# Kernel optimization log

Hardware: AMD Instinct MI355X
Metric: run time of the kernel (lower is better)

## Reference

```python
import jax, jax.numpy as jnp
import numpy as np

IN_CAPS, IN_SIZE = 1152, 8
OUT_CAPS, OUT_SIZE = 10, 16
ROUTING_ITERS = 3
EPS = 1e-8


def squash(s, axis):
    # v = (||s||^2 / (1 + ||s||^2)) * s / ||s||
    sq = jnp.sum(s * s, axis=axis, keepdims=True)
    return (sq / (1.0 + sq)) * s / jnp.sqrt(sq + EPS)


def setup_inputs() -> dict:
    key = jax.random.key(0)
    k1, k2 = jax.random.split(key)
    B = 1024
    x = jax.random.normal(k1, (B, IN_CAPS, IN_SIZE), dtype=jnp.float32)
    W = jax.random.normal(k2, (IN_CAPS, IN_SIZE, OUT_CAPS * OUT_SIZE), dtype=jnp.float32)
    b_ij = jnp.zeros((IN_CAPS, OUT_CAPS), dtype=jnp.float32)
    return {"x": x, "W": W, "b_ij": b_ij}


def reference(x, W, b_ij):
    B = x.shape[0]
    # u_hat[b,i,j,d]: prediction vectors. (B,1152,8) x (1152,8,160) -> (B,1152,160)
    u_hat = jnp.einsum('bis,iso->bio', x, W).reshape(B, IN_CAPS, OUT_CAPS, OUT_SIZE)
    u_hat_d = jax.lax.stop_gradient(u_hat)

    # initial coupling from learned logits b_ij
    c_ij = jax.nn.softmax(b_ij, axis=1)                      # (1152,10)
    s_j = jnp.einsum('ij,bijd->bjd', c_ij, u_hat_d)          # (B,10,16)
    v_j = squash(s_j, axis=2)

    b_batch = jnp.broadcast_to(b_ij, (B, IN_CAPS, OUT_CAPS))
    for it in range(ROUTING_ITERS):
        # agreement: (B,1152,10)
        b_batch = b_batch + jnp.einsum('bijd,bjd->bij', u_hat_d, v_j)
        c = jax.nn.softmax(b_batch, axis=2)                  # (B,1152,10)
        u = u_hat if it == ROUTING_ITERS - 1 else u_hat_d
        s_j = jnp.einsum('bij,bijd->bjd', c, u)              # (B,10,16)
        v_j = squash(s_j, axis=2)
    return v_j
```

## Files before the change

### kernel.cpp

```cpp
#include <hip/hip_runtime.h>

#define IC 1152
#define IS 8
#define OC 10
#define OS 16
#define OD 160
#define SQ_EPS 1e-8f

typedef _Float16 half8 __attribute__((ext_vector_type(8)));
typedef float f32x4 __attribute__((ext_vector_type(4)));


__global__ __launch_bounds__(160) void prep_w(const float* __restrict__ W,
                                              uint4* __restrict__ WF) {
  int cap = blockIdx.x;
  int j = threadIdx.x >> 4;
  int lp = threadIdx.x & 15;
  union { _Float16 h[8]; uint4 u; } pk;
#pragma unroll
  for (int i = 0; i < 8; i++)
    pk.h[i] = (_Float16)W[(size_t)cap * (IS * OD) + i * OD + j * 16 + lp];
  WF[((size_t)cap * OC + j) * 16 + lp] = pk.u;
}

template <bool PASS0>
__global__ __launch_bounds__(256) void pass_mfma(
    const float* __restrict__ x, const uint4* __restrict__ WF,
    const float* __restrict__ bij, const float* __restrict__ Vsum,
    float* __restrict__ s_accum, int Bn) {
  int b0 = blockIdx.x * 16;
  int cap0 = blockIdx.y * 64;
  int tid = threadIdx.x;
  int wid = tid >> 6;
  int lane = tid & 63;
  int bl = lane & 15;
  int og = (lane >> 4) * 4;
  int gb = b0 + bl;
  bool bok = gb < Bn;

  __shared__ __align__(16) uint4 xlh[64 * 16];
  __shared__ float sred[4 * 16 * 161];

  for (int e = tid; e < 64 * 16; e += 256) {
    int cc = e & 63, bb = e >> 6;
    int b = b0 + bb;
    float xf[8] = {0, 0, 0, 0, 0, 0, 0, 0};
    if (b < Bn) {
      *(float4*)&xf[0] = *(const float4*)&x[((size_t)b * IC + cap0 + cc) * IS];
      *(float4*)&xf[4] =
          *(const float4*)&x[((size_t)b * IC + cap0 + cc) * IS + 4];
    }
    union { _Float16 h[8]; uint4 u; } pk;
#pragma unroll
    for (int s = 0; s < 8; s++) pk.h[s] = (_Float16)xf[s];
    xlh[cc * 16 + (bb ^ (cc & 15))] = pk.u;
  }
  __syncthreads();

  f32x4 vs4[OC];
#pragma unroll
  for (int j = 0; j < OC; j++) vs4[j] = (f32x4){0.f, 0.f, 0.f, 0.f};
  if (!PASS0 && bok) {
    const float* vrow = Vsum + (size_t)gb * OD;
#pragma unroll
    for (int j = 0; j < OC; j++) {
      float4 t = *(const float4*)(vrow + j * 16 + og);
      vs4[j] = (f32x4){t.x, t.y, t.z, t.w};
    }
  }

  f32x4 sacc[OC];
#pragma unroll
  for (int j = 0; j < OC; j++) sacc[j] = (f32x4){0.f, 0.f, 0.f, 0.f};

  for (int c = 0; c < 16; ++c) {
    int cc = wid * 16 + c;
    int cap = cap0 + cc;

    union { uint4 u; half8 h; } xb;
    xb.u = xlh[cc * 16 + ((lane < 16 ? lane : 0) ^ (cc & 15))];
    if (lane >= 16) xb.u = make_uint4(0, 0, 0, 0);

    f32x4 uf[OC];
#pragma unroll
    for (int j = 0; j < OC; j++) {
      union { uint4 u; half8 h; } wa;
      wa.u = WF[((size_t)cap * OC + j) * 16 + (lane & 15)];
      if (lane >= 16) wa.u = make_uint4(0, 0, 0, 0);
      f32x4 z = {0.f, 0.f, 0.f, 0.f};
      uf[j] = __builtin_amdgcn_mfma_f32_16x16x32_f16(wa.h, xb.h, z, 0, 0, 0);
    }

    float l[OC];
#pragma unroll
    for (int j = 0; j < OC; j++) {
      float bj = bij[cap * OC + j];
      if (PASS0) {
        l[j] = bj;
      } else {
        float t = uf[j].x * vs4[j].x + uf[j].y * vs4[j].y +
                  uf[j].z * vs4[j].z + uf[j].w * vs4[j].w;
        t += __shfl_xor(t, 16, 64);
        t += __shfl_xor(t, 32, 64);
        l[j] = bj + t;
      }
    }
    float m = l[0];
#pragma unroll
    for (int j = 1; j < OC; j++) m = fmaxf(m, l[j]);
    float sum = 0.f, cexp[OC];
#pragma unroll
    for (int j = 0; j < OC; j++) {
      cexp[j] = __expf(l[j] - m);
      sum += cexp[j];
    }
    float inv = 1.f / sum;
#pragma unroll
    for (int j = 0; j < OC; j++) {
      float cj = cexp[j] * inv;
      sacc[j].x += cj * uf[j].x;
      sacc[j].y += cj * uf[j].y;
      sacc[j].z += cj * uf[j].z;
      sacc[j].w += cj * uf[j].w;
    }
  }

  float* sw = &sred[wid * (16 * 161) + bl * 161];
#pragma unroll
  for (int j = 0; j < OC; j++) {
    sw[j * 16 + og + 0] = sacc[j].x;
    sw[j * 16 + og + 1] = sacc[j].y;
    sw[j * 16 + og + 2] = sacc[j].z;
    sw[j * 16 + og + 3] = sacc[j].w;
  }
  __syncthreads();

  for (int e = tid; e < 16 * OD; e += 256) {
    int bb = e / OD, d = e - bb * OD;
    float s = sred[0 * (16 * 161) + bb * 161 + d] +
              sred[1 * (16 * 161) + bb * 161 + d] +
              sred[2 * (16 * 161) + bb * 161 + d] +
              sred[3 * (16 * 161) + bb * 161 + d];
    int g = b0 + bb;
    if (g < Bn) atomicAdd(&s_accum[(size_t)g * OD + d], s);
  }
}

__global__ __launch_bounds__(192) void reduce_squash_kernel(
    float* __restrict__ s_accum, float* __restrict__ Vsum,
    float* __restrict__ out, int mode) {
  int b = blockIdx.x;
  int tid = threadIdx.x;
  __shared__ float sl[OD];
  __shared__ float sc[OC];
  if (tid < OD) {
    float s = s_accum[(size_t)b * OD + tid];
    s_accum[(size_t)b * OD + tid] = 0.f;
    sl[tid] = s;
  }
  __syncthreads();
  if (tid < OC) {
    float sq = 0.f;
#pragma unroll
    for (int d = 0; d < OS; d++) {
      float v = sl[tid * OS + d];
      sq += v * v;
    }
    sc[tid] = (sq / (1.f + sq)) / sqrtf(sq + SQ_EPS);
  }
  __syncthreads();
  if (tid < OD) {
    float v = sl[tid] * sc[tid >> 4];
    if (mode == 2)
      out[(size_t)b * OD + tid] = v;
    else if (mode == 0)
      Vsum[(size_t)b * OD + tid] = v;
    else
      Vsum[(size_t)b * OD + tid] += v;
  }
}

#define BT 16
#define CPC 8
#define CHUNKS 8
#define CG 18
#define WL_STRIDE 1296
#define XL_STRIDE 68

template <bool PASS0>
__global__ __launch_bounds__(256) void pass_kernel(
    const float* __restrict__ x, const float* __restrict__ W,
    const float* __restrict__ bij, const float* __restrict__ Vsum,
    float* __restrict__ s_accum, int Bn) {
  int b0 = blockIdx.x * BT;
  int capg0 = blockIdx.y * (CPC * CHUNKS);
  int tid = threadIdx.x;
  int dq = tid & 3;
  int ch = (tid >> 2) & 3;
  int bb = tid >> 4;
  int b = b0 + bb;
  bool bok = b < Bn;

  __shared__ __align__(16) float Wl[CPC * WL_STRIDE];
  __shared__ __align__(16) float xl[BT * XL_STRIDE];
  __shared__ float bijl[CPC * CHUNKS * OC];

  for (int a = tid; a < CPC * CHUNKS * OC; a += 256)
    bijl[a] = bij[(size_t)capg0 * OC + a];

  float4 vs[OC];
#pragma unroll
  for (int j = 0; j < OC; j++) {
    if (PASS0 || !bok)
      vs[j] = make_float4(0.f, 0.f, 0.f, 0.f);
    else
      vs[j] = *(const float4*)&Vsum[(size_t)b * OD + j * 16 + dq * 4];
  }

  float4 sacc[OC];
#pragma unroll
  for (int j = 0; j < OC; j++) sacc[j] = make_float4(0.f, 0.f, 0.f, 0.f);

  for (int c = 0; c < CHUNKS; ++c) {
    int cap0 = capg0 + c * CPC;
    __syncthreads();
#pragma unroll
    for (int k = 0; k < 10; k++) {
      int a4 = k * 256 + tid;
      int ci = a4 / 320;
      int r4 = a4 - ci * 320;
      float4 w = *(const float4*)&W[(size_t)cap0 * 1280 + (size_t)a4 * 4];
      *(float4*)&Wl[ci * WL_STRIDE + r4 * 4] = w;
    }
#pragma unroll
    for (int k = 0; k < 4; k++) {
      int a = k * 256 + tid;
      int xb = a >> 6, r = a & 63;
      int gbx = b0 + xb;
      xl[xb * XL_STRIDE + r] =
          (gbx < Bn) ? x[((size_t)gbx * IC + cap0) * IS + r] : 0.f;
    }
    __syncthreads();

#pragma unroll
    for (int it = 0; it < 2; ++it) {
      int ci = it * 4 + ch;
      int cap = cap0 + ci;
      float xf[8];
      *(float4*)&xf[0] = *(const float4*)&xl[bb * XL_STRIDE + ci * 8];
      *(float4*)&xf[4] = *(const float4*)&xl[bb * XL_STRIDE + ci * 8 + 4];

      float4 u[OC];
#pragma unroll
      for (int j = 0; j < OC; j++) {
        float4 acc = make_float4(0.f, 0.f, 0.f, 0.f);
#pragma unroll
        for (int s = 0; s < 8; s++) {
          float4 w =
              *(const float4*)&Wl[ci * WL_STRIDE + s * OD + j * 16 + dq * 4];
          acc.x += xf[s] * w.x;
          acc.y += xf[s] * w.y;
          acc.z += xf[s] * w.z;
          acc.w += xf[s] * w.w;
        }
        u[j] = acc;
      }

      float l[OC];
#pragma unroll
      for (int j = 0; j < OC; j++) {
        float a = u[j].x * vs[j].x + u[j].y * vs[j].y + u[j].z * vs[j].z +
                  u[j].w * vs[j].w;
        a += __shfl_xor(a, 1, 64);
        a += __shfl_xor(a, 2, 64);
        l[j] = bijl[(cap - capg0) * OC + j] + a;
      }
      float m = l[0];
#pragma unroll
      for (int j = 1; j < OC; j++) m = fmaxf(m, l[j]);
      float sum = 0.f, cc2[OC];
#pragma unroll
      for (int j = 0; j < OC; j++) {
        cc2[j] = __expf(l[j] - m);
        sum += cc2[j];
      }
      float inv = 1.f / sum;
#pragma unroll
      for (int j = 0; j < OC; j++) {
        float w = cc2[j] * inv;
        sacc[j].x += w * u[j].x;
        sacc[j].y += w * u[j].y;
        sacc[j].z += w * u[j].z;
        sacc[j].w += w * u[j].w;
      }
    }
  }

#pragma unroll
  for (int mask = 4; mask <= 8; mask <<= 1) {
#pragma unroll
    for (int j = 0; j < OC; j++) {
      sacc[j].x += __shfl_xor(sacc[j].x, mask, 64);
      sacc[j].y += __shfl_xor(sacc[j].y, mask, 64);
      sacc[j].z += __shfl_xor(sacc[j].z, mask, 64);
      sacc[j].w += __shfl_xor(sacc[j].w, mask, 64);
    }
  }
  if (ch == 0 && bok) {
    float* sb = s_accum + (size_t)b * OD + dq * 4;
#pragma unroll
    for (int j = 0; j < OC; j++) {
      atomicAdd(&sb[j * 16 + 0], sacc[j].x);
      atomicAdd(&sb[j * 16 + 1], sacc[j].y);
      atomicAdd(&sb[j * 16 + 2], sacc[j].z);
      atomicAdd(&sb[j * 16 + 3], sacc[j].w);
    }
  }
}

__global__ __launch_bounds__(256) void routing_fallback(
    const float* __restrict__ x, const float* __restrict__ W,
    const float* __restrict__ bij, float* __restrict__ out) {
  int b = blockIdx.x;
  int tid = threadIdx.x;
  int wid = tid >> 6;
  int lane = tid & 63;
  int dq = lane & 3;
  int slot = wid * 16 + (lane >> 2);

  __shared__ __align__(16) float Vs[OD];
  __shared__ __align__(16) float sred2[4][OD];
  __shared__ float sc[OC];

  if (tid < OD) Vs[tid] = 0.f;
  __syncthreads();

  for (int pass = 0; pass < 4; ++pass) {
    float4 vsr[OC];
#pragma unroll
    for (int j = 0; j < OC; j++) vsr[j] = *(const float4*)&Vs[j * 16 + dq * 4];
    float4 sp[OC];
#pragma unroll
    for (int j = 0; j < OC; j++) sp[j] = make_float4(0.f, 0.f, 0.f, 0.f);

    for (int r = 0; r < IC / 64; ++r) {
      int cap = r * 64 + slot;
      float xr[8];
#pragma unroll
      for (int s = 0; s < 8; s++) xr[s] = x[((size_t)b * IC + cap) * IS + s];
      float4 u[OC];
#pragma unroll
      for (int j = 0; j < OC; j++) {
        float4 acc = make_float4(0.f, 0.f, 0.f, 0.f);
#pragma unroll
        for (int s = 0; s < 8; s++) {
          const float4 w =
              *(const float4*)&W[((size_t)cap * IS + s) * OD + j * 16 + dq * 4];
          acc.x += xr[s] * w.x;
          acc.y += xr[s] * w.y;
          acc.z += xr[s] * w.z;
          acc.w += xr[s] * w.w;
        }
        u[j] = acc;
      }
      float l[OC];
#pragma unroll
      for (int j = 0; j < OC; j++) {
        float a = u[j].x * vsr[j].x + u[j].y * vsr[j].y + u[j].z * vsr[j].z +
                  u[j].w * vsr[j].w;
        a += __shfl_xor(a, 1, 64);
        a += __shfl_xor(a, 2, 64);
        l[j] = bij[cap * OC + j] + a;
      }
      float m = l[0];
#pragma unroll
      for (int j = 1; j < OC; j++) m = fmaxf(m, l[j]);
      float sum = 0.f, c[OC];
#pragma unroll
      for (int j = 0; j < OC; j++) {
        c[j] = __expf(l[j] - m);
        sum += c[j];
      }
      float inv = 1.f / sum;
#pragma unroll
      for (int j = 0; j < OC; j++) {
        float ccv = c[j] * inv;
        sp[j].x += ccv * u[j].x;
        sp[j].y += ccv * u[j].y;
        sp[j].z += ccv * u[j].z;
        sp[j].w += ccv * u[j].w;
      }
    }
#pragma unroll
    for (int mask = 4; mask <= 32; mask <<= 1) {
#pragma unroll
      for (int j = 0; j < OC; j++) {
        sp[j].x += __shfl_xor(sp[j].x, mask, 64);
        sp[j].y += __shfl_xor(sp[j].y, mask, 64);
        sp[j].z += __shfl_xor(sp[j].z, mask, 64);
        sp[j].w += __shfl_xor(sp[j].w, mask, 64);
      }
    }
    if (lane < 4) {
#pragma unroll
      for (int j = 0; j < OC; j++)
        *(float4*)&sred2[wid][j * 16 + dq * 4] = sp[j];
    }
    __syncthreads();
    if (tid < OD) {
      float s = sred2[0][tid] + sred2[1][tid] + sred2[2][tid] + sred2[3][tid];
      sred2[0][tid] = s;
    }
    __syncthreads();
    if (tid < OC) {
      float sq = 0.f;
#pragma unroll
      for (int d = 0; d < OS; d++) {
        float v = sred2[0][tid * OS + d];
        sq += v * v;
      }
      sc[tid] = (sq / (1.f + sq)) / sqrtf(sq + SQ_EPS);
    }
    __syncthreads();
    if (tid < OD) {
      float vv = sred2[0][tid] * sc[tid >> 4];
      if (pass < 3)
        Vs[tid] += vv;
      else
        out[(size_t)b * OD + tid] = vv;
    }
    __syncthreads();
  }
}

extern "C" void kernel_launch(void* const* d_in, const int* in_sizes, int n_in,
                              void* d_out, int out_size, void* d_ws,
                              size_t ws_size, hipStream_t stream) {
  const float* x = (const float*)d_in[0];
  const float* W = (const float*)d_in[1];
  const float* bij = (const float*)d_in[2];
  float* out = (float*)d_out;

  int Bn = in_sizes[0] / (IC * IS);
  size_t buf = (size_t)Bn * OD * sizeof(float);
  size_t wf_bytes = (size_t)IC * OC * 16 * 16;

  if (ws_size >= wf_bytes + 2 * buf) {
    uint4* WF = (uint4*)d_ws;
    float* s_accum = (float*)((char*)d_ws + wf_bytes);
    float* Vs = (float*)((char*)d_ws + wf_bytes + buf);

    prep_w<<<IC, 160, 0, stream>>>(W, WF);
    hipMemsetAsync(s_accum, 0, buf, stream);

    dim3 pg((Bn + 15) / 16, IC / 64);
    pass_mfma<true><<<pg, 256, 0, stream>>>(x, WF, bij, nullptr, s_accum, Bn);
    reduce_squash_kernel<<<Bn, 192, 0, stream>>>(s_accum, Vs, out, 0);
    pass_mfma<false><<<pg, 256, 0, stream>>>(x, WF, bij, Vs, s_accum, Bn);
    reduce_squash_kernel<<<Bn, 192, 0, stream>>>(s_accum, Vs, out, 1);
    pass_mfma<false><<<pg, 256, 0, stream>>>(x, WF, bij, Vs, s_accum, Bn);
    reduce_squash_kernel<<<Bn, 192, 0, stream>>>(s_accum, Vs, out, 1);
    pass_mfma<false><<<pg, 256, 0, stream>>>(x, WF, bij, Vs, s_accum, Bn);
    reduce_squash_kernel<<<Bn, 192, 0, stream>>>(s_accum, Vs, out, 2);
  } else if (ws_size >= 2 * buf) {
    float* s_accum = (float*)d_ws;
    float* Vs = (float*)((char*)d_ws + buf);
    hipMemsetAsync(s_accum, 0, buf, stream);
    dim3 pg((Bn + BT - 1) / BT, CG);
    pass_kernel<true><<<pg, 256, 0, stream>>>(x, W, bij, nullptr, s_accum, Bn);
    reduce_squash_kernel<<<Bn, 192, 0, stream>>>(s_accum, Vs, out, 0);
    pass_kernel<false><<<pg, 256, 0, stream>>>(x, W, bij, Vs, s_accum, Bn);
    reduce_squash_kernel<<<Bn, 192, 0, stream>>>(s_accum, Vs, out, 1);
    pass_kernel<false><<<pg, 256, 0, stream>>>(x, W, bij, Vs, s_accum, Bn);
    reduce_squash_kernel<<<Bn, 192, 0, stream>>>(s_accum, Vs, out, 1);
    pass_kernel<false><<<pg, 256, 0, stream>>>(x, W, bij, Vs, s_accum, Bn);
    reduce_squash_kernel<<<Bn, 192, 0, stream>>>(s_accum, Vs, out, 2);
  } else {
    routing_fallback<<<Bn, 256, 0, stream>>>(x, W, bij, out);
  }
}
```

Before: 262.8 us.

## Replace global atomics with per-chunk partial sums reduced in squash kernel

Each pass block now writes its per-chunk partial sum into a dedicated slot of an s_part buffer instead of doing global atomicAdd into s_accum. The squash kernel sums the 18 partials, which removes the memset and the global atomic contention. Inside the block, the four per-wave shared buffers become one shared buffer accumulated with LDS atomics, which lowers LDS usage. The redundant zeroing of W fragments for upper lanes is dropped, and the non-MFMA fp32 path is deleted, so smaller workspaces fall to the slow fallback.

```diff
diff --git a/kernel.cpp b/kernel.cpp
--- a/kernel.cpp
+++ b/kernel.cpp
@@ -6,10 +6,11 @@
 #define OS 16
 #define OD 160
 #define SQ_EPS 1e-8f
+#define NCH 18
+#define SRED_STRIDE 165
 
 typedef _Float16 half8 __attribute__((ext_vector_type(8)));
 typedef float f32x4 __attribute__((ext_vector_type(4)));
-
 
 __global__ __launch_bounds__(160) void prep_w(const float* __restrict__ W,
                                               uint4* __restrict__ WF) {
@@ -27,9 +28,10 @@
 __global__ __launch_bounds__(256) void pass_mfma(
     const float* __restrict__ x, const uint4* __restrict__ WF,
     const float* __restrict__ bij, const float* __restrict__ Vsum,
-    float* __restrict__ s_accum, int Bn) {
+    float* __restrict__ s_part, int Bn) {
   int b0 = blockIdx.x * 16;
-  int cap0 = blockIdx.y * 64;
+  int ch = blockIdx.y;
+  int cap0 = ch * 64;
   int tid = threadIdx.x;
   int wid = tid >> 6;
   int lane = tid & 63;
@@ -39,7 +41,9 @@
   bool bok = gb < Bn;
 
   __shared__ __align__(16) uint4 xlh[64 * 16];
-  __shared__ float sred[4 * 16 * 161];
+  __shared__ float sred[16 * SRED_STRIDE];
+
+  for (int e = tid; e < 16 * SRED_STRIDE; e += 256) sred[e] = 0.f;
 
   for (int e = tid; e < 64 * 16; e += 256) {
     int cc = e & 63, bb = e >> 6;
@@ -86,7 +90,6 @@
     for (int j = 0; j < OC; j++) {
       union { uint4 u; half8 h; } wa;
       wa.u = WF[((size_t)cap * OC + j) * 16 + (lane & 15)];
-      if (lane >= 16) wa.u = make_uint4(0, 0, 0, 0);
       f32x4 z = {0.f, 0.f, 0.f, 0.f};
       uf[j] = __builtin_amdgcn_mfma_f32_16x16x32_f16(wa.h, xb.h, z, 0, 0, 0);
     }
@@ -125,37 +128,36 @@
     }
   }
 
-  float* sw = &sred[wid * (16 * 161) + bl * 161];
+  float* sw = &sred[bl * SRED_STRIDE];
 #pragma unroll
   for (int j = 0; j < OC; j++) {
-    sw[j * 16 + og + 0] = sacc[j].x;
-    sw[j * 16 + og + 1] = sacc[j].y;
-    sw[j * 16 + og + 2] = sacc[j].z;
-    sw[j * 16 + og + 3] = sacc[j].w;
+    atomicAdd(&sw[j * 16 + og + 0], sacc[j].x);
+    atomicAdd(&sw[j * 16 + og + 1], sacc[j].y);
+    atomicAdd(&sw[j * 16 + og + 2], sacc[j].z);
+    atomicAdd(&sw[j * 16 + og + 3], sacc[j].w);
   }
   __syncthreads();
 
   for (int e = tid; e < 16 * OD; e += 256) {
     int bb = e / OD, d = e - bb * OD;
-    float s = sred[0 * (16 * 161) + bb * 161 + d] +
-              sred[1 * (16 * 161) + bb * 161 + d] +
-              sred[2 * (16 * 161) + bb * 161 + d] +
-              sred[3 * (16 * 161) + bb * 161 + d];
     int g = b0 + bb;
-    if (g < Bn) atomicAdd(&s_accum[(size_t)g * OD + d], s);
-  }
-}
-
-__global__ __launch_bounds__(192) void reduce_squash_kernel(
-    float* __restrict__ s_accum, float* __restrict__ Vsum,
+    if (g < Bn)
+      s_part[((size_t)g * NCH + ch) * OD + d] = sred[bb * SRED_STRIDE + d];
+  }
+}
+
+__global__ __launch_bounds__(192) void reduce_squash_part(
+    const float* __restrict__ s_part, float* __restrict__ Vsum,
     float* __restrict__ out, int mode) {
   int b = blockIdx.x;
   int tid = threadIdx.x;
   __shared__ float sl[OD];
   __shared__ float sc[OC];
   if (tid < OD) {
-    float s = s_accum[(size_t)b * OD + tid];
-    s_accum[(size_t)b * OD + tid] = 0.f;
+    float s = 0.f;
+#pragma unroll
+    for (int chk = 0; chk < NCH; chk++)
+      s += s_part[((size_t)b * NCH + chk) * OD + tid];
     sl[tid] = s;
   }
   __syncthreads();
@@ -177,144 +179,6 @@
       Vsum[(size_t)b * OD + tid] = v;
     else
       Vsum[(size_t)b * OD + tid] += v;
-  }
-}
-
-#define BT 16
-#define CPC 8
-#define CHUNKS 8
-#define CG 18
-#define WL_STRIDE 1296
-#define XL_STRIDE 68
-
-template <bool PASS0>
-__global__ __launch_bounds__(256) void pass_kernel(
-    const float* __restrict__ x, const float* __restrict__ W,
-    const float* __restrict__ bij, const float* __restrict__ Vsum,
-    float* __restrict__ s_accum, int Bn) {
-  int b0 = blockIdx.x * BT;
-  int capg0 = blockIdx.y * (CPC * CHUNKS);
-  int tid = threadIdx.x;
-  int dq = tid & 3;
-  int ch = (tid >> 2) & 3;
-  int bb = tid >> 4;
-  int b = b0 + bb;
-  bool bok = b < Bn;
-
-  __shared__ __align__(16) float Wl[CPC * WL_STRIDE];
-  __shared__ __align__(16) float xl[BT * XL_STRIDE];
-  __shared__ float bijl[CPC * CHUNKS * OC];
-
-  for (int a = tid; a < CPC * CHUNKS * OC; a += 256)
-    bijl[a] = bij[(size_t)capg0 * OC + a];
-
-  float4 vs[OC];
-#pragma unroll
-  for (int j = 0; j < OC; j++) {
-    if (PASS0 || !bok)
-      vs[j] = make_float4(0.f, 0.f, 0.f, 0.f);
-    else
-      vs[j] = *(const float4*)&Vsum[(size_t)b * OD + j * 16 + dq * 4];
-  }
-
-  float4 sacc[OC];
-#pragma unroll
-  for (int j = 0; j < OC; j++) sacc[j] = make_float4(0.f, 0.f, 0.f, 0.f);
-
-  for (int c = 0; c < CHUNKS; ++c) {
-    int cap0 = capg0 + c * CPC;
-    __syncthreads();
-#pragma unroll
-    for (int k = 0; k < 10; k++) {
-      int a4 = k * 256 + tid;
-      int ci = a4 / 320;
-      int r4 = a4 - ci * 320;
-      float4 w = *(const float4*)&W[(size_t)cap0 * 1280 + (size_t)a4 * 4];
-      *(float4*)&Wl[ci * WL_STRIDE + r4 * 4] = w;
-    }
-#pragma unroll
-    for (int k = 0; k < 4; k++) {
-      int a = k * 256 + tid;
-      int xb = a >> 6, r = a & 63;
-      int gbx = b0 + xb;
-      xl[xb * XL_STRIDE + r] =
-          (gbx < Bn) ? x[((size_t)gbx * IC + cap0) * IS + r] : 0.f;
-    }
-    __syncthreads();
-
-#pragma unroll
-    for (int it = 0; it < 2; ++it) {
-      int ci = it * 4 + ch;
-      int cap = cap0 + ci;
-      float xf[8];
-      *(float4*)&xf[0] = *(const float4*)&xl[bb * XL_STRIDE + ci * 8];
-      *(float4*)&xf[4] = *(const float4*)&xl[bb * XL_STRIDE + ci * 8 + 4];
-
-      float4 u[OC];
-#pragma unroll
-      for (int j = 0; j < OC; j++) {
-        float4 acc = make_float4(0.f, 0.f, 0.f, 0.f);
-#pragma unroll
-        for (int s = 0; s < 8; s++) {
-          float4 w =
-              *(const float4*)&Wl[ci * WL_STRIDE + s * OD + j * 16 + dq * 4];
-          acc.x += xf[s] * w.x;
-          acc.y += xf[s] * w.y;
-          acc.z += xf[s] * w.z;
-          acc.w += xf[s] * w.w;
-        }
-        u[j] = acc;
-      }
-
-      float l[OC];
-#pragma unroll
-      for (int j = 0; j < OC; j++) {
-        float a = u[j].x * vs[j].x + u[j].y * vs[j].y + u[j].z * vs[j].z +
-                  u[j].w * vs[j].w;
-        a += __shfl_xor(a, 1, 64);
-        a += __shfl_xor(a, 2, 64);
-        l[j] = bijl[(cap - capg0) * OC + j] + a;
-      }
-      float m = l[0];
-#pragma unroll
-      for (int j = 1; j < OC; j++) m = fmaxf(m, l[j]);
-      float sum = 0.f, cc2[OC];
-#pragma unroll
-      for (int j = 0; j < OC; j++) {
-        cc2[j] = __expf(l[j] - m);
-        sum += cc2[j];
-      }
-      float inv = 1.f / sum;
-#pragma unroll
-      for (int j = 0; j < OC; j++) {
-        float w = cc2[j] * inv;
-        sacc[j].x += w * u[j].x;
-        sacc[j].y += w * u[j].y;
-        sacc[j].z += w * u[j].z;
-        sacc[j].w += w * u[j].w;
-      }
-    }
-  }
-
-#pragma unroll
-  for (int mask = 4; mask <= 8; mask <<= 1) {
-#pragma unroll
-    for (int j = 0; j < OC; j++) {
-      sacc[j].x += __shfl_xor(sacc[j].x, mask, 64);
-      sacc[j].y += __shfl_xor(sacc[j].y, mask, 64);
-      sacc[j].z += __shfl_xor(sacc[j].z, mask, 64);
-      sacc[j].w += __shfl_xor(sacc[j].w, mask, 64);
-    }
-  }
-  if (ch == 0 && bok) {
-    float* sb = s_accum + (size_t)b * OD + dq * 4;
-#pragma unroll
-    for (int j = 0; j < OC; j++) {
-      atomicAdd(&sb[j * 16 + 0], sacc[j].x);
-      atomicAdd(&sb[j * 16 + 1], sacc[j].y);
-      atomicAdd(&sb[j * 16 + 2], sacc[j].z);
-      atomicAdd(&sb[j * 16 + 3], sacc[j].w);
-    }
   }
 }
 
@@ -444,37 +308,24 @@
   int Bn = in_sizes[0] / (IC * IS);
   size_t buf = (size_t)Bn * OD * sizeof(float);
   size_t wf_bytes = (size_t)IC * OC * 16 * 16;
-
-  if (ws_size >= wf_bytes + 2 * buf) {
+  size_t spart_bytes = (size_t)Bn * NCH * OD * sizeof(float);
+
+  if (ws_size >= wf_bytes + spart_bytes + buf) {
     uint4* WF = (uint4*)d_ws;
-    float* s_accum = (float*)((char*)d_ws + wf_bytes);
-    float* Vs = (float*)((char*)d_ws + wf_bytes + buf);
+    float* s_part = (float*)((char*)d_ws + wf_bytes);
+    float* Vs = (float*)((char*)d_ws + wf_bytes + spart_bytes);
 
     prep_w<<<IC, 160, 0, stream>>>(W, WF);
-    hipMemsetAsync(s_accum, 0, buf, stream);
-
-    dim3 pg((Bn + 15) / 16, IC / 64);
-    pass_mfma<true><<<pg, 256, 0, stream>>>(x, WF, bij, nullptr, s_accum, Bn);
-    reduce_squash_kernel<<<Bn, 192, 0, stream>>>(s_accum, Vs, out, 0);
-    pass_mfma<false><<<pg, 256, 0, stream>>>(x, WF, bij, Vs, s_accum, Bn);
-    reduce_squash_kernel<<<Bn, 192, 0, stream>>>(s_accum, Vs, out, 1);
-    pass_mfma<false><<<pg, 256, 0, stream>>>(x, WF, bij, Vs, s_accum, Bn);
-    reduce_squash_kernel<<<Bn, 192, 0, stream>>>(s_accum, Vs, out, 1);
-    pass_mfma<false><<<pg, 256, 0, stream>>>(x, WF, bij, Vs, s_accum, Bn);
-    reduce_squash_kernel<<<Bn, 192, 0, stream>>>(s_accum, Vs, out, 2);
-  } else if (ws_size >= 2 * buf) {
-    float* s_accum = (float*)d_ws;
-    float* Vs = (float*)((char*)d_ws + buf);
-    hipMemsetAsync(s_accum, 0, buf, stream);
-    dim3 pg((Bn + BT - 1) / BT, CG);
-    pass_kernel<true><<<pg, 256, 0, stream>>>(x, W, bij, nullptr, s_accum, Bn);
-    reduce_squash_kernel<<<Bn, 192, 0, stream>>>(s_accum, Vs, out, 0);
-    pass_kernel<false><<<pg, 256, 0, stream>>>(x, W, bij, Vs, s_accum, Bn);
-    reduce_squash_kernel<<<Bn, 192, 0, stream>>>(s_accum, Vs, out, 1);
-    pass_kernel<false><<<pg, 256, 0, stream>>>(x, W, bij, Vs, s_accum, Bn);
-    reduce_squash_kernel<<<Bn, 192, 0, stream>>>(s_accum, Vs, out, 1);
-    pass_kernel<false><<<pg, 256, 0, stream>>>(x, W, bij, Vs, s_accum, Bn);
-    reduce_squash_kernel<<<Bn, 192, 0, stream>>>(s_accum, Vs, out, 2);
+
+    dim3 pg((Bn + 15) / 16, NCH);
+    pass_mfma<true><<<pg, 256, 0, stream>>>(x, WF, bij, nullptr, s_part, Bn);
+    reduce_squash_part<<<Bn, 192, 0, stream>>>(s_part, Vs, out, 0);
+    pass_mfma<false><<<pg, 256, 0, stream>>>(x, WF, bij, Vs, s_part, Bn);
+    reduce_squash_part<<<Bn, 192, 0, stream>>>(s_part, Vs, out, 1);
+    pass_mfma<false><<<pg, 256, 0, stream>>>(x, WF, bij, Vs, s_part, Bn);
+    reduce_squash_part<<<Bn, 192, 0, stream>>>(s_part, Vs, out, 1);
+    pass_mfma<false><<<pg, 256, 0, stream>>>(x, WF, bij, Vs, s_part, Bn);
+    reduce_squash_part<<<Bn, 192, 0, stream>>>(s_part, Vs, out, 2);
   } else {
     routing_fallback<<<Bn, 256, 0, stream>>>(x, W, bij, out);
   }
```

Result: slower. 524.5 us (+99.6%).
